# Performance work log

Hardware: AMD Instinct MI355X
Metric: run time of the kernel (lower is better)

## Reference

```python
import jax, jax.numpy as jnp
import numpy as np

N = 8192
C_IN = 128
C_OUT = 128
E = 262144


def setup_inputs() -> dict:
    key = jax.random.key(0)
    ks = jax.random.split(key, 8)
    x = jax.random.normal(ks[0], (1, C_IN, N), dtype=jnp.float32)
    edge_index = jax.random.randint(ks[1], (2, E), 0, N, dtype=jnp.int64)
    adj_mat = jax.random.randint(ks[2], (N, N), 0, 2).astype(jnp.float32)
    # conv1: Conv1d(C_IN, C_OUT, k=1, bias=False) -> weight (C_OUT, C_IN)
    W1 = jax.random.normal(ks[3], (C_OUT, C_IN), dtype=jnp.float32) * (1.0 / np.sqrt(C_IN))
    # f1/f2: Conv1d(C_OUT, 1, k=1) -> weight (C_OUT,), bias scalar
    w_f1 = jax.random.normal(ks[4], (C_OUT,), dtype=jnp.float32) * (1.0 / np.sqrt(C_OUT))
    b_f1 = jnp.zeros((), dtype=jnp.float32)
    w_f2 = jax.random.normal(ks[5], (C_OUT,), dtype=jnp.float32) * (1.0 / np.sqrt(C_OUT))
    b_f2 = jnp.zeros((), dtype=jnp.float32)
    return {"x": x, "edge_index": edge_index, "adj_mat": adj_mat,
            "W1": W1, "w_f1": w_f1, "b_f1": b_f1, "w_f2": w_f2, "b_f2": b_f2}


def reference(x, edge_index, adj_mat, W1, w_f1, b_f1, w_f2, b_f2):
    # seq_fts = conv1(x): 1x1 conv == GEMM over channel dim. (C_OUT, N)
    seq_fts = jnp.einsum('oc,cn->on', W1, x[0])
    # f1/f2: 1x1 conv to single channel -> per-node attention scalars (N,)
    a1 = jnp.einsum('c,cn->n', w_f1, seq_fts) + b_f1
    a2 = jnp.einsum('c,cn->n', w_f2, seq_fts) + b_f2
    # logits = adj*f1 + adj*f2^T  (N, N)
    logits = adj_mat * a1[:, None] + adj_mat * a2[None, :]
    coefs = jax.nn.softmax(jax.nn.leaky_relu(logits, negative_slope=0.01), axis=-1)
    # vals = coefs @ seq_fts^T  (N, C_OUT)
    vals = jnp.matmul(coefs, seq_fts.T)
    return jax.nn.elu(vals)[None]  # (1, N, C_OUT)
```

## Files before the change

kernel.cpp:

```cpp
#include <hip/hip_runtime.h>
#include <hip/hip_bf16.h>


typedef short bf16x8 __attribute__((ext_vector_type(8)));
typedef float f32x4 __attribute__((ext_vector_type(4)));

static __device__ __forceinline__ short f2bf(float f) {
  union { float f; unsigned u; } v; v.f = f;
  unsigned r = v.u + 0x7fffu + ((v.u >> 16) & 1u);
  return (short)(r >> 16);
}

static __device__ __forceinline__ void gld16(const short* g, short* l) {
  __builtin_amdgcn_global_load_lds(
      (const __attribute__((address_space(1))) void*)g,
      (__attribute__((address_space(3))) void*)l, 16, 0, 0);
}

__global__ __launch_bounds__(256) void k1_seqfts(
    const float* __restrict__ x, const float* __restrict__ W1,
    const float* __restrict__ wf1, const float* __restrict__ wf2,
    short* __restrict__ FT, float* __restrict__ a1, float* __restrict__ a2) {
  const int cb = blockIdx.x & 7;
  const int nb = blockIdx.x >> 3;
  const int n = nb * 256 + threadIdx.x;
  float acc[16];
#pragma unroll
  for (int i = 0; i < 16; ++i) acc[i] = 0.f;
  const float* wrow = W1 + cb * 16 * 128;
#pragma unroll 4
  for (int c = 0; c < 128; ++c) {
    float xv = x[c * 8192 + n];
#pragma unroll
    for (int cc = 0; cc < 16; ++cc) acc[cc] = fmaf(wrow[cc * 128 + c], xv, acc[cc]);
  }
  float p1 = 0.f, p2 = 0.f;
#pragma unroll
  for (int cc = 0; cc < 16; ++cc) {
    int co = cb * 16 + cc;
    FT[co * 8192 + n] = f2bf(acc[cc]);
    p1 = fmaf(wf1[co], acc[cc], p1);
    p2 = fmaf(wf2[co], acc[cc], p2);
  }
  atomicAdd(&a1[n], p1);
  atomicAdd(&a2[n], p2);
}

__global__ __launch_bounds__(512, 2) void k2_attn(
    const float* __restrict__ adj, const short* __restrict__ FT,
    const float* __restrict__ a1, const float* __restrict__ a2,
    const float* __restrict__ b1p, const float* __restrict__ b2p,
    float* __restrict__ out) {
  __shared__ __align__(16) short Pl[2][4360];
  __shared__ __align__(16) short Ftl[2][16384];
  __shared__ float zl[32];

  const int t = threadIdx.x;
  const int l = t & 63;
  const int w = t >> 6;
  const int r = l & 15;
  const int kg = l >> 4;
  const int i0 = blockIdx.x * 32;

  const int prow = t >> 4;
  const int pcg = t & 15;
  const float af = a1[i0 + prow] + b1p[0] + b2p[0];
  const float* adjp = adj + (size_t)(i0 + prow) * 8192 + pcg * 8;
  const float* a2p = a2 + pcg * 8;

  const int swz = 8 * (r ^ ((w * 4 + kg) & 15));
  const short* fsrc0 = FT + (size_t)(0 + w * 4 + kg) * 8192 + swz;
  const short* fsrc1 = FT + (size_t)(32 + w * 4 + kg) * 8192 + swz;
  const short* fsrc2 = FT + (size_t)(64 + w * 4 + kg) * 8192 + swz;
  const short* fsrc3 = FT + (size_t)(96 + w * 4 + kg) * 8192 + swz;

  const int mt = w >> 2;
  const int ct0 = (w & 3) * 2;
  const int arow = mt * 16 + r;
  const int c0 = ct0 * 16 + r;

  f32x4 acc0 = {0.f, 0.f, 0.f, 0.f};
  f32x4 acc1 = {0.f, 0.f, 0.f, 0.f};
  float zacc = 0.f;

  auto build = [&](int buf, const f32x4& A0, const f32x4& A1,
                   const f32x4& Q0, const f32x4& Q1) {
    bf16x8 pv;
#pragma unroll
    for (int j = 0; j < 4; ++j) {
      float tt = af + Q0[j];
      float lr = fmaxf(tt, 0.01f * tt);
      float p = __expf(A0[j] * lr);
      zacc += p;
      pv[j] = f2bf(p);
    }
#pragma unroll
    for (int j = 0; j < 4; ++j) {
      float tt = af + Q1[j];
      float lr = fmaxf(tt, 0.01f * tt);
      float p = __expf(A1[j] * lr);
      zacc += p;
      pv[4 + j] = f2bf(p);
    }
    *(bf16x8*)&Pl[buf][prow * 136 + pcg * 8] = pv;
  };

  auto compute = [&](int cur) {
    const short* pb = &Pl[cur][arow * 136 + kg * 8];
    const short* fb = &Ftl[cur][0];
#pragma unroll
    for (int kt = 0; kt < 4; ++kt) {
      const int koff = (kg * 8 + kt * 32) ^ (r * 8);
      bf16x8 Af = *(const bf16x8*)(pb + kt * 32);
      bf16x8 B0 = *(const bf16x8*)(fb + c0 * 128 + koff);
      bf16x8 B1 = *(const bf16x8*)(fb + (c0 + 16) * 128 + koff);
      acc0 = __builtin_amdgcn_mfma_f32_16x16x32_bf16(Af, B0, acc0, 0, 0, 0);
      acc1 = __builtin_amdgcn_mfma_f32_16x16x32_bf16(Af, B1, acc1, 0, 0, 0);
    }
  };

  auto body = [&](int s, const f32x4& uA0, const f32x4& uA1,
                  const f32x4& uQ0, const f32x4& uQ1,
                  f32x4& fA0, f32x4& fA1, f32x4& fQ0, f32x4& fQ1) {
    const int cur = s & 1, nxt = cur ^ 1;
    if (s + 1 < 64) {
      const int kb1 = (s + 1) * 128;
      short* fb = &Ftl[nxt][w * 512];
      gld16(fsrc0 + kb1, fb);
      gld16(fsrc1 + kb1, fb + 4096);
      gld16(fsrc2 + kb1, fb + 8192);
      gld16(fsrc3 + kb1, fb + 12288);
    }
    if (s + 2 < 64) {
      const int kb2 = (s + 2) * 128;
      fA0 = *(const f32x4*)(adjp + kb2);
      fA1 = *(const f32x4*)(adjp + kb2 + 4);
      fQ0 = *(const f32x4*)(a2p + kb2);
      fQ1 = *(const f32x4*)(a2p + kb2 + 4);
    }
    if (s + 1 < 64) build(nxt, uA0, uA1, uQ0, uQ1);
    compute(cur);
    __syncthreads();
  };

  {
    short* fb = &Ftl[0][w * 512];
    gld16(fsrc0, fb);
    gld16(fsrc1, fb + 4096);
    gld16(fsrc2, fb + 8192);
    gld16(fsrc3, fb + 12288);
  }
  f32x4 tA0 = *(const f32x4*)(adjp);
  f32x4 tA1 = *(const f32x4*)(adjp + 4);
  f32x4 tQ0 = *(const f32x4*)(a2p);
  f32x4 tQ1 = *(const f32x4*)(a2p + 4);
  f32x4 oA0 = *(const f32x4*)(adjp + 128);
  f32x4 oA1 = *(const f32x4*)(adjp + 132);
  f32x4 oQ0 = *(const f32x4*)(a2p + 128);
  f32x4 oQ1 = *(const f32x4*)(a2p + 132);
  f32x4 eA0 = {0, 0, 0, 0}, eA1 = {0, 0, 0, 0}, eQ0 = {0, 0, 0, 0}, eQ1 = {0, 0, 0, 0};
  build(0, tA0, tA1, tQ0, tQ1);
  __syncthreads();

  for (int s = 0; s < 64; s += 2) {
    body(s, oA0, oA1, oQ0, oQ1, eA0, eA1, eQ0, eQ1);
    body(s + 1, eA0, eA1, eQ0, eQ1, oA0, oA1, oQ0, oQ1);
  }

  float zr = zacc;
  zr += __shfl_down(zr, 8, 16);
  zr += __shfl_down(zr, 4, 16);
  zr += __shfl_down(zr, 2, 16);
  zr += __shfl_down(zr, 1, 16);
  if (pcg == 0) zl[prow] = zr;
  __syncthreads();

#pragma unroll
  for (int q = 0; q < 4; ++q) {
    const int row = mt * 16 + kg * 4 + q;
    const float inv = 1.0f / zl[row];
    float v0 = acc0[q] * inv;
    v0 = v0 > 0.f ? v0 : __expf(v0) - 1.f;
    out[(size_t)(i0 + row) * 128 + c0] = v0;
    float v1 = acc1[q] * inv;
    v1 = v1 > 0.f ? v1 : __expf(v1) - 1.f;
    out[(size_t)(i0 + row) * 128 + c0 + 16] = v1;
  }
}

extern "C" void kernel_launch(void* const* d_in, const int* in_sizes, int n_in,
                              void* d_out, int out_size, void* d_ws, size_t ws_size,
                              hipStream_t stream) {
  const float* x   = (const float*)d_in[0];
  const float* adj = (const float*)d_in[2];
  const float* W1  = (const float*)d_in[3];
  const float* wf1 = (const float*)d_in[4];
  const float* b1  = (const float*)d_in[5];
  const float* wf2 = (const float*)d_in[6];
  const float* b2  = (const float*)d_in[7];
  float* out = (float*)d_out;

  short* FT = (short*)d_ws;
  float* a1 = (float*)((char*)d_ws + (size_t)2 * 1024 * 1024);
  float* a2 = a1 + 8192;

  hipMemsetAsync(a1, 0, 2 * 8192 * sizeof(float), stream);
  k1_seqfts<<<256, 256, 0, stream>>>(x, W1, wf1, wf2, FT, a1, a2);
  k2_attn<<<256, 512, 0, stream>>>(adj, FT, a1, a2, b1, b2, out);
}
```

Measured before the change: 104.5 us.

## Halve attention row tile to 16 rows and double grid to 512 blocks

The attention kernel now handles 16 query rows per block instead of 32, launches 512 blocks, and raises the occupancy hint to 4 blocks per CU. Each wave computes one 16x16 output tile rather than two, and each thread builds 4 probabilities per step instead of 8. The goal is to spread the memory-bound adjacency stream over more CUs (256 blocks roughly matched the CU count) and keep more waves in flight. The cost is that every block reloads the full seq_fts matrix through LDS, so that traffic doubles while each load is reused for only one MFMA tile.

Result: slower. 116.1 us (+11.2%).

```diff
diff --git a/kernel.cpp b/kernel.cpp
--- a/kernel.cpp
+++ b/kernel.cpp
@@ -46,27 +46,27 @@
   atomicAdd(&a2[n], p2);
 }
 
-__global__ __launch_bounds__(512, 2) void k2_attn(
+__global__ __launch_bounds__(512, 4) void k2_attn(
     const float* __restrict__ adj, const short* __restrict__ FT,
     const float* __restrict__ a1, const float* __restrict__ a2,
     const float* __restrict__ b1p, const float* __restrict__ b2p,
     float* __restrict__ out) {
-  __shared__ __align__(16) short Pl[2][4360];
+  __shared__ __align__(16) short Pl[2][16 * 136];
   __shared__ __align__(16) short Ftl[2][16384];
-  __shared__ float zl[32];
+  __shared__ float zl[16];
 
   const int t = threadIdx.x;
   const int l = t & 63;
   const int w = t >> 6;
   const int r = l & 15;
   const int kg = l >> 4;
-  const int i0 = blockIdx.x * 32;
+  const int i0 = blockIdx.x * 16;
 
-  const int prow = t >> 4;
-  const int pcg = t & 15;
+  const int prow = t >> 5;
+  const int pcg = t & 31;
   const float af = a1[i0 + prow] + b1p[0] + b2p[0];
-  const float* adjp = adj + (size_t)(i0 + prow) * 8192 + pcg * 8;
-  const float* a2p = a2 + pcg * 8;
+  const float* adjp = adj + (size_t)(i0 + prow) * 8192 + pcg * 4;
+  const float* a2p = a2 + pcg * 4;
 
   const int swz = 8 * (r ^ ((w * 4 + kg) & 15));
   const short* fsrc0 = FT + (size_t)(0 + w * 4 + kg) * 8192 + swz;
@@ -74,54 +74,37 @@
   const short* fsrc2 = FT + (size_t)(64 + w * 4 + kg) * 8192 + swz;
   const short* fsrc3 = FT + (size_t)(96 + w * 4 + kg) * 8192 + swz;
 
-  const int mt = w >> 2;
-  const int ct0 = (w & 3) * 2;
-  const int arow = mt * 16 + r;
-  const int c0 = ct0 * 16 + r;
+  const int c0 = w * 16 + r;
 
-  f32x4 acc0 = {0.f, 0.f, 0.f, 0.f};
-  f32x4 acc1 = {0.f, 0.f, 0.f, 0.f};
+  f32x4 acc = {0.f, 0.f, 0.f, 0.f};
   float zacc = 0.f;
 
-  auto build = [&](int buf, const f32x4& A0, const f32x4& A1,
-                   const f32x4& Q0, const f32x4& Q1) {
-    bf16x8 pv;
-#pragma unroll
-    for (int j = 0; j < 4; ++j) {
-      float tt = af + Q0[j];
-      float lr = fmaxf(tt, 0.01f * tt);
-      float p = __expf(A0[j] * lr);
-      zacc += p;
-      pv[j] = f2bf(p);
-    }
-#pragma unroll
-    for (int j = 0; j < 4; ++j) {
-      float tt = af + Q1[j];
-      float lr = fmaxf(tt, 0.01f * tt);
-      float p = __expf(A1[j] * lr);
-      zacc += p;
-      pv[4 + j] = f2bf(p);
-    }
-    *(bf16x8*)&Pl[buf][prow * 136 + pcg * 8] = pv;
+  auto build = [&](int buf, const f32x4& A, const f32x4& Q) {
+    ushort4 pv;
+    float tt, lr, p;
+    tt = af + Q[0]; lr = fmaxf(tt, 0.01f * tt); p = __expf(A[0] * lr);
+    zacc += p; pv.x = (unsigned short)f2bf(p);
+    tt = af + Q[1]; lr = fmaxf(tt, 0.01f * tt); p = __expf(A[1] * lr);
+    zacc += p; pv.y = (unsigned short)f2bf(p);
+    tt = af + Q[2]; lr = fmaxf(tt, 0.01f * tt); p = __expf(A[2] * lr);
+    zacc += p; pv.z = (unsigned short)f2bf(p);
+    tt = af + Q[3]; lr = fmaxf(tt, 0.01f * tt); p = __expf(A[3] * lr);
+    zacc += p; pv.w = (unsigned short)f2bf(p);
+    *(ushort4*)&Pl[buf][prow * 136 + pcg * 4] = pv;
   };
 
   auto compute = [&](int cur) {
-    const short* pb = &Pl[cur][arow * 136 + kg * 8];
-    const short* fb = &Ftl[cur][0];
+    const short* pb = &Pl[cur][r * 136 + kg * 8];
+    const short* fb = &Ftl[cur][c0 * 128];
 #pragma unroll
     for (int kt = 0; kt < 4; ++kt) {
-      const int koff = (kg * 8 + kt * 32) ^ (r * 8);
       bf16x8 Af = *(const bf16x8*)(pb + kt * 32);
-      bf16x8 B0 = *(const bf16x8*)(fb + c0 * 128 + koff);
-      bf16x8 B1 = *(const bf16x8*)(fb + (c0 + 16) * 128 + koff);
-      acc0 = __builtin_amdgcn_mfma_f32_16x16x32_bf16(Af, B0, acc0, 0, 0, 0);
-      acc1 = __builtin_amdgcn_mfma_f32_16x16x32_bf16(Af, B1, acc1, 0, 0, 0);
+      bf16x8 Bf = *(const bf16x8*)(fb + ((kg * 8 + kt * 32) ^ (r * 8)));
+      acc = __builtin_amdgcn_mfma_f32_16x16x32_bf16(Af, Bf, acc, 0, 0, 0);
     }
   };
 
-  auto body = [&](int s, const f32x4& uA0, const f32x4& uA1,
-                  const f32x4& uQ0, const f32x4& uQ1,
-                  f32x4& fA0, f32x4& fA1, f32x4& fQ0, f32x4& fQ1) {
+  auto body = [&](int s, const f32x4& uA, const f32x4& uQ, f32x4& fA, f32x4& fQ) {
     const int cur = s & 1, nxt = cur ^ 1;
     if (s + 1 < 64) {
       const int kb1 = (s + 1) * 128;
@@ -133,12 +116,10 @@
     }
     if (s + 2 < 64) {
       const int kb2 = (s + 2) * 128;
-      fA0 = *(const f32x4*)(adjp + kb2);
-      fA1 = *(const f32x4*)(adjp + kb2 + 4);
-      fQ0 = *(const f32x4*)(a2p + kb2);
-      fQ1 = *(const f32x4*)(a2p + kb2 + 4);
+      fA = *(const f32x4*)(adjp + kb2);
+      fQ = *(const f32x4*)(a2p + kb2);
     }
-    if (s + 1 < 64) build(nxt, uA0, uA1, uQ0, uQ1);
+    if (s + 1 < 64) build(nxt, uA, uQ);
     compute(cur);
     __syncthreads();
   };
@@ -150,41 +131,35 @@
     gld16(fsrc2, fb + 8192);
     gld16(fsrc3, fb + 12288);
   }
-  f32x4 tA0 = *(const f32x4*)(adjp);
-  f32x4 tA1 = *(const f32x4*)(adjp + 4);
-  f32x4 tQ0 = *(const f32x4*)(a2p);
-  f32x4 tQ1 = *(const f32x4*)(a2p + 4);
-  f32x4 oA0 = *(const f32x4*)(adjp + 128);
-  f32x4 oA1 = *(const f32x4*)(adjp + 132);
-  f32x4 oQ0 = *(const f32x4*)(a2p + 128);
-  f32x4 oQ1 = *(const f32x4*)(a2p + 132);
-  f32x4 eA0 = {0, 0, 0, 0}, eA1 = {0, 0, 0, 0}, eQ0 = {0, 0, 0, 0}, eQ1 = {0, 0, 0, 0};
-  build(0, tA0, tA1, tQ0, tQ1);
+  f32x4 tA = *(const f32x4*)(adjp);
+  f32x4 tQ = *(const f32x4*)(a2p);
+  f32x4 oA = *(const f32x4*)(adjp + 128);
+  f32x4 oQ = *(const f32x4*)(a2p + 128);
+  f32x4 eA = {0, 0, 0, 0}, eQ = {0, 0, 0, 0};
+  build(0, tA, tQ);
   __syncthreads();
 
   for (int s = 0; s < 64; s += 2) {
-    body(s, oA0, oA1, oQ0, oQ1, eA0, eA1, eQ0, eQ1);
-    body(s + 1, eA0, eA1, eQ0, eQ1, oA0, oA1, oQ0, oQ1);
+    body(s, oA, oQ, eA, eQ);
+    body(s + 1, eA, eQ, oA, oQ);
   }
 
   float zr = zacc;
-  zr += __shfl_down(zr, 8, 16);
-  zr += __shfl_down(zr, 4, 16);
-  zr += __shfl_down(zr, 2, 16);
-  zr += __shfl_down(zr, 1, 16);
+  zr += __shfl_down(zr, 16, 32);
+  zr += __shfl_down(zr, 8, 32);
+  zr += __shfl_down(zr, 4, 32);
+  zr += __shfl_down(zr, 2, 32);
+  zr += __shfl_down(zr, 1, 32);
   if (pcg == 0) zl[prow] = zr;
   __syncthreads();
 
 #pragma unroll
   for (int q = 0; q < 4; ++q) {
-    const int row = mt * 16 + kg * 4 + q;
+    const int row = kg * 4 + q;
     const float inv = 1.0f / zl[row];
-    float v0 = acc0[q] * inv;
-    v0 = v0 > 0.f ? v0 : __expf(v0) - 1.f;
-    out[(size_t)(i0 + row) * 128 + c0] = v0;
-    float v1 = acc1[q] * inv;
-    v1 = v1 > 0.f ? v1 : __expf(v1) - 1.f;
-    out[(size_t)(i0 + row) * 128 + c0 + 16] = v1;
+    float v = acc[q] * inv;
+    v = v > 0.f ? v : __expf(v) - 1.f;
+    out[(size_t)(i0 + row) * 128 + c0] = v;
   }
 }
 
@@ -206,5 +181,5 @@
 
   hipMemsetAsync(a1, 0, 2 * 8192 * sizeof(float), stream);
   k1_seqfts<<<256, 256, 0, stream>>>(x, W1, wf1, wf2, FT, a1, a2);
-  k2_attn<<<256, 512, 0, stream>>>(adj, FT, a1, a2, b1, b2, out);
+  k2_attn<<<512, 512, 0, stream>>>(adj, FT, a1, a2, b1, b2, out);
 }
```

## Triple-buffer feature tiles with prefetch distance two and manual waitcnt barriers

Applied to the files above, without the earlier changes.

Moves the LDS staging of the bf16 feature tiles from double to triple buffering, so each tile is prefetched two steps ahead instead of one. `__syncthreads` is replaced by an explicit `s_waitcnt lgkmcnt(0)`, a partial `vmcnt(4)` and a raw `s_barrier`. This lets the newest feature prefetch stay in flight across the barrier, while the adjacency and a2 loads and the older stage must complete. Scheduling barriers pin the order of loads, staging, softmax build and MFMA compute. The aim is to hide global-load latency behind compute, at the cost of extra LDS and fragile hand-written wait counts.

New measurement: 116.7 us. 1.12x slower.

```diff
diff --git a/kernel.cpp b/kernel.cpp
--- a/kernel.cpp
+++ b/kernel.cpp
@@ -51,8 +51,8 @@
     const float* __restrict__ a1, const float* __restrict__ a2,
     const float* __restrict__ b1p, const float* __restrict__ b2p,
     float* __restrict__ out) {
+  __shared__ __align__(16) short Ftl[3][16384];
   __shared__ __align__(16) short Pl[2][4360];
-  __shared__ __align__(16) short Ftl[2][16384];
   __shared__ float zl[32];
 
   const int t = threadIdx.x;
@@ -83,6 +83,15 @@
   f32x4 acc1 = {0.f, 0.f, 0.f, 0.f};
   float zacc = 0.f;
 
+  auto STAGE = [&](int s) {
+    const int kb = s * 128;
+    short* fb = &Ftl[s % 3][w * 512];
+    gld16(fsrc0 + kb, fb);
+    gld16(fsrc1 + kb, fb + 4096);
+    gld16(fsrc2 + kb, fb + 8192);
+    gld16(fsrc3 + kb, fb + 12288);
+  };
+
   auto build = [&](int buf, const f32x4& A0, const f32x4& A1,
                    const f32x4& Q0, const f32x4& Q1) {
     bf16x8 pv;
@@ -105,9 +114,9 @@
     *(bf16x8*)&Pl[buf][prow * 136 + pcg * 8] = pv;
   };
 
-  auto compute = [&](int cur) {
-    const short* pb = &Pl[cur][arow * 136 + kg * 8];
-    const short* fb = &Ftl[cur][0];
+  auto compute = [&](int pbuf, int fbuf) {
+    const short* pb = &Pl[pbuf][arow * 136 + kg * 8];
+    const short* fb = &Ftl[fbuf][0];
 #pragma unroll
     for (int kt = 0; kt < 4; ++kt) {
       const int koff = (kg * 8 + kt * 32) ^ (r * 8);
@@ -122,15 +131,7 @@
   auto body = [&](int s, const f32x4& uA0, const f32x4& uA1,
                   const f32x4& uQ0, const f32x4& uQ1,
                   f32x4& fA0, f32x4& fA1, f32x4& fQ0, f32x4& fQ1) {
-    const int cur = s & 1, nxt = cur ^ 1;
-    if (s + 1 < 64) {
-      const int kb1 = (s + 1) * 128;
-      short* fb = &Ftl[nxt][w * 512];
-      gld16(fsrc0 + kb1, fb);
-      gld16(fsrc1 + kb1, fb + 4096);
-      gld16(fsrc2 + kb1, fb + 8192);
-      gld16(fsrc3 + kb1, fb + 12288);
-    }
+    __builtin_amdgcn_sched_barrier(0);
     if (s + 2 < 64) {
       const int kb2 = (s + 2) * 128;
       fA0 = *(const f32x4*)(adjp + kb2);
@@ -138,18 +139,23 @@
       fQ0 = *(const f32x4*)(a2p + kb2);
       fQ1 = *(const f32x4*)(a2p + kb2 + 4);
     }
-    if (s + 1 < 64) build(nxt, uA0, uA1, uQ0, uQ1);
-    compute(cur);
-    __syncthreads();
-  };
-
-  {
-    short* fb = &Ftl[0][w * 512];
-    gld16(fsrc0, fb);
-    gld16(fsrc1, fb + 4096);
-    gld16(fsrc2, fb + 8192);
-    gld16(fsrc3, fb + 12288);
-  }
+    __builtin_amdgcn_sched_barrier(0);
+    if (s + 2 < 64) STAGE(s + 2);
+    __builtin_amdgcn_sched_barrier(0);
+    if (s + 1 < 64) build((s + 1) & 1, uA0, uA1, uQ0, uQ1);
+    compute(s & 1, s % 3);
+    asm volatile("s_waitcnt lgkmcnt(0)" ::: "memory");
+    if (s < 62) {
+      asm volatile("s_waitcnt vmcnt(4)" ::: "memory");
+    } else {
+      asm volatile("s_waitcnt vmcnt(0)" ::: "memory");
+    }
+    __builtin_amdgcn_s_barrier();
+  };
+
+  STAGE(0);
+  STAGE(1);
+  __builtin_amdgcn_sched_barrier(0);
   f32x4 tA0 = *(const f32x4*)(adjp);
   f32x4 tA1 = *(const f32x4*)(adjp + 4);
   f32x4 tQ0 = *(const f32x4*)(a2p);
@@ -158,14 +164,17 @@
   f32x4 oA1 = *(const f32x4*)(adjp + 132);
   f32x4 oQ0 = *(const f32x4*)(a2p + 128);
   f32x4 oQ1 = *(const f32x4*)(a2p + 132);
+  __builtin_amdgcn_sched_barrier(0);
+  build(0, tA0, tA1, tQ0, tQ1);
   f32x4 eA0 = {0, 0, 0, 0}, eA1 = {0, 0, 0, 0}, eQ0 = {0, 0, 0, 0}, eQ1 = {0, 0, 0, 0};
-  build(0, tA0, tA1, tQ0, tQ1);
-  __syncthreads();
+  asm volatile("s_waitcnt lgkmcnt(0)" ::: "memory");
+  __builtin_amdgcn_s_barrier();
 
   for (int s = 0; s < 64; s += 2) {
     body(s, oA0, oA1, oQ0, oQ1, eA0, eA1, eQ0, eQ1);
     body(s + 1, eA0, eA1, eQ0, eQ1, oA0, oA1, oQ0, oQ1);
   }
+  __builtin_amdgcn_sched_barrier(0);
 
   float zr = zacc;
   zr += __shfl_down(zr, 8, 16);
```
